# Performance work log

Measured on AMD Instinct MI355X. Metric: run time of the kernel, lower is better.

Reference implementation:

```python
import jax, jax.numpy as jnp
import numpy as np

CI_SCALE = 1.0


def _rot_y(a):
    c, s = np.cos(a), np.sin(a)
    return np.array([[c, 0.0, s], [0.0, 1.0, 0.0], [-s, 0.0, c]], dtype=np.float32)


def setup_inputs() -> dict:
    key = jax.random.key(0)
    B, V, C, Hs, Ws = 1, 3, 32, 256, 256
    Ht, Wt, D = 128, 128, 48
    src_feat = jax.random.normal(key, (B, V, C, Hs, Ws), dtype=jnp.float32)
    # Realistic pinhole cameras so the plane-sweep warp lands in-frame.
    Ks = np.array([[200.0, 0.0, Ws / 2], [0.0, 200.0, Hs / 2], [0.0, 0.0, 1.0]], dtype=np.float32)
    Kt = np.array([[100.0, 0.0, Wt / 2], [0.0, 100.0, Ht / 2], [0.0, 0.0, 1.0]], dtype=np.float32)
    src_exts = np.zeros((B, V, 4, 4), dtype=np.float32)
    for i in range(V):
        R = _rot_y(0.1 * (i - (V - 1) / 2))
        src_exts[0, i, :3, :3] = R
        src_exts[0, i, :3, 3] = np.array([-0.3 * (i - (V - 1) / 2), 0.0, 0.0], dtype=np.float32)
        src_exts[0, i, 3, 3] = 1.0
    tar_exts = np.eye(4, dtype=np.float32)[None]
    return {
        "src_feat": src_feat,
        "src_exts": jnp.asarray(src_exts),
        "src_ints": jnp.asarray(np.broadcast_to(Ks, (B, V, 3, 3)).copy()),
        "tar_exts": jnp.asarray(tar_exts),
        "tar_ints": jnp.asarray(Kt[None].copy()),
        "near_far": jnp.broadcast_to(jnp.array([2.0, 6.0], dtype=jnp.float32).reshape(1, 2, 1, 1), (B, 2, Ht, Wt)),
        "num_depth": D,
    }


def _grid_sample_zeros(feat, grid):
    """Bilinear, padding_mode='zeros', align_corners=False.
    feat: (N,C,Hs,Ws); grid: (N,Hg,Wg,2) normalized -> (N,C,Hg,Wg)."""
    N, C, Hs, Ws = feat.shape
    gx = jnp.clip((grid[..., 0] + 1.0) * (Ws / 2) - 0.5, -1e6, 1e6)
    gy = jnp.clip((grid[..., 1] + 1.0) * (Hs / 2) - 0.5, -1e6, 1e6)
    x0f, y0f = jnp.floor(gx), jnp.floor(gy)
    wx, wy = gx - x0f, gy - y0f
    x0, y0 = x0f.astype(jnp.int32), y0f.astype(jnp.int32)
    x1, y1 = x0 + 1, y0 + 1
    b = jnp.arange(N)[:, None, None]

    def tap(yi, xi):
        valid = (xi >= 0) & (xi < Ws) & (yi >= 0) & (yi < Hs)
        v = feat[b, :, jnp.clip(yi, 0, Hs - 1), jnp.clip(xi, 0, Ws - 1)]  # (N,Hg,Wg,C)
        return v * valid[..., None]

    out = (tap(y0, x0) * ((1 - wy) * (1 - wx))[..., None]
           + tap(y0, x1) * ((1 - wy) * wx)[..., None]
           + tap(y1, x0) * (wy * (1 - wx))[..., None]
           + tap(y1, x1) * (wy * wx)[..., None])
    return jnp.transpose(out, (0, 3, 1, 2))


def _build_feature_volume(src_feat, src_exts, src_ints, tar_exts, tar_ints, depth_values):
    B, V, C, Hs, Ws = src_feat.shape
    D, Ht, Wt = depth_values.shape[1:]
    src_projs = src_ints @ src_exts[..., :3, :]                       # (B,V,3,4)
    tar34 = tar_ints @ tar_exts[:, :3, :]                             # (B,3,4)
    bottom = jnp.broadcast_to(jnp.array([0.0, 0.0, 0.0, 1.0], dtype=tar34.dtype).reshape(1, 1, 4), (B, 1, 4))
    tar_proj = jnp.concatenate([tar34, bottom], axis=1)               # (B,4,4)
    proj = (src_projs @ jnp.linalg.inv(tar_proj)[:, None]).reshape(B * V, 3, 4)
    xs = jnp.arange(Wt, dtype=src_feat.dtype) + 0.5
    ys = jnp.arange(Ht, dtype=src_feat.dtype) + 0.5
    gx, gy = jnp.meshgrid(xs, ys, indexing='xy')                      # (Ht,Wt)
    xyz = jnp.stack([gx, gy, jnp.ones_like(gx)], 0).reshape(3, Ht * Wt)
    dvals = jnp.broadcast_to(depth_values.reshape(B, 1, D, Ht * Wt), (B, V, D, Ht * Wt)).reshape(B * V, 1, D, Ht * Wt)
    p = proj[:, :, :3] @ xyz                                          # (BV,3,HW)
    p = p[:, :, None, :] * dvals + proj[:, :, 3:, None]               # (BV,3,D,HW)
    p = jnp.transpose(p, (0, 2, 3, 1))                                # (BV,D,HW,3)
    z = jnp.maximum(p[..., 2:3], 1e-6)
    g = p[..., :2] / z
    grid = jnp.stack([2 * g[..., 0] / Ws - 1, 2 * g[..., 1] / Hs - 1], -1)  # (BV,D,HW,2)
    warped = _grid_sample_zeros(src_feat.reshape(B * V, C, Hs, Ws), grid)   # (BV,C,D,HW)
    warped = warped.reshape(B, V, C, D, Ht, Wt)
    return jnp.var(warped, axis=1)                                    # (B,C,D,Ht,Wt), unbiased=False


def reference(src_feat, src_exts, src_ints, tar_exts, tar_ints, near_far, num_depth):
    B, _, Ht, Wt = near_far.shape
    t = jnp.linspace(0.0, 1.0, num_depth, dtype=near_far.dtype).reshape(1, num_depth, 1, 1)
    depth_values = near_far[:, :1] + (near_far[:, -1:] - near_far[:, :1]) * t   # (B,D,Ht,Wt)
    vol = _build_feature_volume(src_feat, src_exts, src_ints, tar_exts, tar_ints, depth_values)
    prob = jax.nn.softmax(-vol.mean(axis=1), axis=1)                  # (B,D,Ht,Wt)
    depth = jnp.sum(prob * depth_values, axis=1, keepdims=True)       # (B,1,Ht,Wt)
    var = jnp.sum(prob * jnp.square(depth_values - depth), axis=1, keepdims=True)
    half_ci = CI_SCALE * jnp.sqrt(jnp.maximum(var, 1e-12))
    ci = jnp.concatenate([jnp.maximum(depth - half_ci, depth_values[:, :1]),
                          jnp.minimum(depth + half_ci, depth_values[:, -1:])], axis=1)
    return depth, ci
```

## Files before the change

### kernel.cpp

```cpp
#include <hip/hip_runtime.h>
#include <math.h>

#define NV 3
#define NC 32
#define HS 256
#define WS 256
#define HT 128
#define WT 128
#define ND 48
#define NPIX (HT*WT)
#define HSP 259
#define WSP 259
#define ROW4 (WSP*8)
#define IMG4 (HSP*ROW4)
#define FEAT_T_ELEMS (NV*IMG4*4)
#define NB_INTERIOR (NV*HS)
#define NBORDER_PIX (3*(3*WSP + 3*HS))
#define NBORDER_F4  (NBORDER_PIX*8)
#define NB_BORDER   145

__device__ __forceinline__ float dpp_sum8(float x) {
    int v;
    v = __builtin_amdgcn_update_dpp(0, __float_as_int(x), 0xB1,  0xF, 0xF, true);
    x += __int_as_float(v);
    v = __builtin_amdgcn_update_dpp(0, __float_as_int(x), 0x4E,  0xF, 0xF, true);
    x += __int_as_float(v);
    v = __builtin_amdgcn_update_dpp(0, __float_as_int(x), 0x141, 0xF, 0xF, true);
    x += __int_as_float(v);
    return x;
}
__device__ __forceinline__ float dpp_max8(float x) {
    int v;
    v = __builtin_amdgcn_update_dpp(0, __float_as_int(x), 0xB1,  0xF, 0xF, true);
    x = fmaxf(x, __int_as_float(v));
    v = __builtin_amdgcn_update_dpp(0, __float_as_int(x), 0x4E,  0xF, 0xF, true);
    x = fmaxf(x, __int_as_float(v));
    v = __builtin_amdgcn_update_dpp(0, __float_as_int(x), 0x141, 0xF, 0xF, true);
    x = fmaxf(x, __int_as_float(v));
    return x;
}

__global__ __launch_bounds__(256) void prep(
        const float* __restrict__ src, float* __restrict__ dstf,
        const float* __restrict__ src_exts,
        const float* __restrict__ src_ints,
        const float* __restrict__ tar_exts,
        const float* __restrict__ tar_ints,
        float* __restrict__ proj_out) {
    float4* dst = (float4*)dstf;
    int bid = blockIdx.x;
    if (bid < NB_INTERIOR) {
        int v  = bid >> 8;
        int y  = bid & 255;
        int x0 = threadIdx.x & 31;
        int q  = threadIdx.x >> 5;
        const float* in = src + ((size_t)(v*NC + q*4))*HS*WS + (size_t)y*WS;
        float4* drow = dst + (size_t)(v*HSP + y+1)*ROW4 + 8 + q;
        #pragma unroll
        for (int it = 0; it < 8; it++) {
            int x = it*32 + x0;
            float a = in[x];
            float b = in[HS*WS   + x];
            float c = in[2*HS*WS + x];
            float d = in[3*HS*WS + x];
            drow[x*8] = make_float4(a,b,c,d);
        }
        return;
    }
    int t = (bid - NB_INTERIOR)*256 + threadIdx.x;
    if (t < NBORDER_F4) {
        int pixb = t >> 3, q = t & 7;
        int v = pixb / (NBORDER_PIX/3);
        int r = pixb - v*(NBORDER_PIX/3);
        int y, x;
        if (r < 3*WSP) {
            int band = r / WSP;
            y = (band == 0) ? 0 : (band == 1 ? 257 : 258);
            x = r - band*WSP;
        } else {
            int rr = r - 3*WSP;
            int band = rr >> 8;
            x = (band == 0) ? 0 : (band == 1 ? 257 : 258);
            y = 1 + (rr & 255);
        }
        dst[(v*HSP + y)*WSP*8 + x*8 + q] = make_float4(0.f,0.f,0.f,0.f);
    }
    if (bid == NB_INTERIOR && threadIdx.x == 0) {
        float Kt[9], Et[16];
        for (int i = 0; i < 9;  i++) Kt[i] = tar_ints[i];
        for (int i = 0; i < 16; i++) Et[i] = tar_exts[i];
        float T[12];
        for (int rI = 0; rI < 3; rI++)
            for (int col = 0; col < 4; col++) {
                float s = 0.f;
                for (int k = 0; k < 3; k++) s += Kt[rI*3+k] * Et[k*4+col];
                T[rI*4+col] = s;
            }
        float M[9]  = {T[0],T[1],T[2], T[4],T[5],T[6], T[8],T[9],T[10]};
        float tv[3] = {T[3],T[7],T[11]};
        float det = M[0]*(M[4]*M[8]-M[5]*M[7])
                  - M[1]*(M[3]*M[8]-M[5]*M[6])
                  + M[2]*(M[3]*M[7]-M[4]*M[6]);
        float id = 1.0f/det;
        float Mi[9];
        Mi[0] =  (M[4]*M[8]-M[5]*M[7])*id;
        Mi[1] = -(M[1]*M[8]-M[2]*M[7])*id;
        Mi[2] =  (M[1]*M[5]-M[2]*M[4])*id;
        Mi[3] = -(M[3]*M[8]-M[5]*M[6])*id;
        Mi[4] =  (M[0]*M[8]-M[2]*M[6])*id;
        Mi[5] = -(M[0]*M[5]-M[2]*M[3])*id;
        Mi[6] =  (M[3]*M[7]-M[4]*M[6])*id;
        Mi[7] = -(M[0]*M[7]-M[1]*M[6])*id;
        Mi[8] =  (M[0]*M[4]-M[1]*M[3])*id;
        float mt[3];
        for (int rI = 0; rI < 3; rI++)
            mt[rI] = -(Mi[rI*3+0]*tv[0] + Mi[rI*3+1]*tv[1] + Mi[rI*3+2]*tv[2]);
        float inv4[16] = {Mi[0],Mi[1],Mi[2],mt[0],
                          Mi[3],Mi[4],Mi[5],mt[1],
                          Mi[6],Mi[7],Mi[8],mt[2],
                          0.f,0.f,0.f,1.f};
        for (int v = 0; v < NV; v++) {
            const float* Ks = src_ints + v*9;
            const float* Ev = src_exts + v*16;
            float P34[12];
            for (int rI = 0; rI < 3; rI++)
                for (int col = 0; col < 4; col++) {
                    float s = 0.f;
                    for (int k = 0; k < 3; k++) s += Ks[rI*3+k] * Ev[k*4+col];
                    P34[rI*4+col] = s;
                }
            for (int rI = 0; rI < 3; rI++)
                for (int col = 0; col < 4; col++) {
                    float s = 0.f;
                    for (int k = 0; k < 4; k++) s += P34[rI*4+k] * inv4[k*4+col];
                    proj_out[v*12 + rI*4 + col] = s;
                }
        }
    }
}

__global__ __launch_bounds__(256, 6) void depth_main(
        const float4* __restrict__ featT,
        const float* __restrict__ proj,
        const float* __restrict__ near_far,
        float* __restrict__ out) {
    __shared__ float cl[8][56];

    const int tid  = threadIdx.x;
    const int w    = tid >> 6;
    const int lane = tid & 63;
    const int p    = lane >> 3;
    const int q    = lane & 7;

    const int lb  = ((blockIdx.x & 7) << 8) | (blockIdx.x >> 3);
    const int pix = lb*8 + p;
    const float cx = (pix & (WT-1)) + 0.5f;
    const float cy = (pix >> 7) + 0.5f;

    float rx[NV], ry[NV], rz[NV], tx[NV], ty[NV], tz[NV];
    #pragma unroll
    for (int v = 0; v < NV; v++) {
        const float* P = proj + v*12;
        rx[v] = P[0]*cx + P[1]*cy + P[2];  tx[v] = P[3];
        ry[v] = P[4]*cx + P[5]*cy + P[6];  ty[v] = P[7];
        rz[v] = P[8]*cx + P[9]*cy + P[10]; tz[v] = P[11];
    }

    const float nearv = near_far[pix];
    const float farv  = near_far[NPIX + pix];
    const float step  = (farv - nearv) * (1.0f/(ND-1));
    const float d0    = (float)(w*12);

    const float4* base0 = featT + q;

    #pragma unroll 2
    for (int dd = 0; dd < 12; dd++) {
        const float dv = fmaf(step, d0 + (float)dd, nearv);
        float ax=0.f, ay=0.f, az=0.f, aw=0.f;
        float mxs=0.f, mys=0.f, mzs=0.f, mws=0.f;
        #pragma unroll
        for (int v = 0; v < NV; v++) {
            float pxx = fmaf(rx[v], dv, tx[v]);
            float pyy = fmaf(ry[v], dv, ty[v]);
            float pzz = fmaf(rz[v], dv, tz[v]);
            float z    = fmaxf(pzz, 1e-6f);
            float invz = 1.0f / z;
            float sx = fminf(fmaxf(fmaf(pxx, invz, -0.5f), -1.0f), 256.0f);
            float sy = fminf(fmaxf(fmaf(pyy, invz, -0.5f), -1.0f), 256.0f);
            float x0f = floorf(sx), y0f = floorf(sy);
            float wx = sx - x0f,   wy = sy - y0f;
            int xi = (int)x0f + 1;
            int yi = (int)y0f + 1;
            int r0 = v*IMG4 + yi*ROW4 + xi*8;
            int r1 = r0 + ROW4;
            float4 f00 = base0[r0];
            float4 f01 = base0[r0 + 8];
            float4 f10 = base0[r1];
            float4 f11 = base0[r1 + 8];
            float w11 = wx*wy;
            float w10 = wy - w11;
            float w01 = wx - w11;
            float w00 = (1.0f - wx) - w10;
            float vx = f00.x*w00 + f01.x*w01 + f10.x*w10 + f11.x*w11;
            float vy = f00.y*w00 + f01.y*w01 + f10.y*w10 + f11.y*w11;
            float vz = f00.z*w00 + f01.z*w01 + f10.z*w10 + f11.z*w11;
            float vw = f00.w*w00 + f01.w*w01 + f10.w*w10 + f11.w*w11;
            ax = fmaf(vx,vx,ax); ay = fmaf(vy,vy,ay);
            az = fmaf(vz,vz,az); aw = fmaf(vw,vw,aw);
            mxs += vx; mys += vy; mzs += vz; mws += vw;
        }
        float a  = dpp_sum8((ax + ay) + (az + aw));
        float m2 = dpp_sum8(mxs*mxs + mys*mys + mzs*mzs + mws*mws);
        float cost = (a*(1.0f/3.0f) - m2*(1.0f/9.0f)) * (1.0f/32.0f);
        if (q == 0) cl[p][w*12 + dd] = cost;
    }

    __syncthreads();
    if (w != 0) return;

    float n[6], dvs[6];
    #pragma unroll
    for (int j = 0; j < 6; j++) {
        n[j]   = -cl[p][q + 8*j];
        dvs[j] = fmaf(step, (float)(q + 8*j), nearv);
    }
    float mx = n[0];
    #pragma unroll
    for (int j = 1; j < 6; j++) mx = fmaxf(mx, n[j]);
    mx = dpp_max8(mx);
    float e[6];
    float s0 = 0.f, s1 = 0.f;
    #pragma unroll
    for (int j = 0; j < 6; j++) {
        e[j] = __expf(n[j] - mx);
        s0 += e[j];
        s1 = fmaf(e[j], dvs[j], s1);
    }
    s0 = dpp_sum8(s0);
    s1 = dpp_sum8(s1);
    float depth = s1 / s0;
    float s2 = 0.f;
    #pragma unroll
    for (int j = 0; j < 6; j++) {
        float qd = dvs[j] - depth;
        s2 = fmaf(e[j]*qd, qd, s2);
    }
    s2 = dpp_sum8(s2);
    float var = s2 / s0;
    float hci = sqrtf(fmaxf(var, 1e-12f));
    if (q == 0) {
        out[pix]          = depth;
        out[NPIX + pix]   = fmaxf(depth - hci, nearv);
        out[2*NPIX + pix] = fminf(depth + hci, farv);
    }
}

extern "C" void kernel_launch(void* const* d_in, const int* in_sizes, int n_in,
                              void* d_out, int out_size, void* d_ws, size_t ws_size,
                              hipStream_t stream) {
    const float* src_feat = (const float*)d_in[0];
    const float* src_exts = (const float*)d_in[1];
    const float* src_ints = (const float*)d_in[2];
    const float* tar_exts = (const float*)d_in[3];
    const float* tar_ints = (const float*)d_in[4];
    const float* near_far = (const float*)d_in[5];
    float* out   = (float*)d_out;
    float* featT = (float*)d_ws;
    float* proj  = featT + FEAT_T_ELEMS;

    hipLaunchKernelGGL(prep, dim3(NB_INTERIOR + NB_BORDER), dim3(256), 0, stream,
                       src_feat, featT, src_exts, src_ints, tar_exts, tar_ints, proj);
    hipLaunchKernelGGL(depth_main, dim3(NPIX/8), dim3(256), 0, stream,
                       (const float4*)featT, proj, near_far, out);
}
```

Measured before the change: 123.9 us.

## Use four lanes per pixel with eight channels each in depth kernel

The depth kernel now maps 4 lanes to each pixel, with each lane gathering two adjacent float4s per bilinear tap, so it handles 16 pixels per block. This cuts the DPP reduction steps and raises per-lane ILP, but costs more registers, so the launch bounds drop from 6 to 4 blocks. The softmax stage now reads 12 depth costs per lane. The prep transpose remaps threads so that consecutive lanes write consecutive float4s. The division is replaced by a hardware reciprocal.

```diff
diff --git a/kernel.cpp b/kernel.cpp
--- a/kernel.cpp
+++ b/kernel.cpp
@@ -19,23 +19,19 @@
 #define NBORDER_F4  (NBORDER_PIX*8)
 #define NB_BORDER   145
 
-__device__ __forceinline__ float dpp_sum8(float x) {
+__device__ __forceinline__ float dpp_sum4(float x) {
     int v;
-    v = __builtin_amdgcn_update_dpp(0, __float_as_int(x), 0xB1,  0xF, 0xF, true);
+    v = __builtin_amdgcn_update_dpp(0, __float_as_int(x), 0xB1, 0xF, 0xF, true);
     x += __int_as_float(v);
-    v = __builtin_amdgcn_update_dpp(0, __float_as_int(x), 0x4E,  0xF, 0xF, true);
-    x += __int_as_float(v);
-    v = __builtin_amdgcn_update_dpp(0, __float_as_int(x), 0x141, 0xF, 0xF, true);
+    v = __builtin_amdgcn_update_dpp(0, __float_as_int(x), 0x4E, 0xF, 0xF, true);
     x += __int_as_float(v);
     return x;
 }
-__device__ __forceinline__ float dpp_max8(float x) {
+__device__ __forceinline__ float dpp_max4(float x) {
     int v;
-    v = __builtin_amdgcn_update_dpp(0, __float_as_int(x), 0xB1,  0xF, 0xF, true);
+    v = __builtin_amdgcn_update_dpp(0, __float_as_int(x), 0xB1, 0xF, 0xF, true);
     x = fmaxf(x, __int_as_float(v));
-    v = __builtin_amdgcn_update_dpp(0, __float_as_int(x), 0x4E,  0xF, 0xF, true);
-    x = fmaxf(x, __int_as_float(v));
-    v = __builtin_amdgcn_update_dpp(0, __float_as_int(x), 0x141, 0xF, 0xF, true);
+    v = __builtin_amdgcn_update_dpp(0, __float_as_int(x), 0x4E, 0xF, 0xF, true);
     x = fmaxf(x, __int_as_float(v));
     return x;
 }
@@ -52,13 +48,13 @@
     if (bid < NB_INTERIOR) {
         int v  = bid >> 8;
         int y  = bid & 255;
-        int x0 = threadIdx.x & 31;
-        int q  = threadIdx.x >> 5;
+        int q  = threadIdx.x & 7;
+        int xl = threadIdx.x >> 3;
         const float* in = src + ((size_t)(v*NC + q*4))*HS*WS + (size_t)y*WS;
         float4* drow = dst + (size_t)(v*HSP + y+1)*ROW4 + 8 + q;
         #pragma unroll
         for (int it = 0; it < 8; it++) {
-            int x = it*32 + x0;
+            int x = it*32 + xl;
             float a = in[x];
             float b = in[HS*WS   + x];
             float c = in[2*HS*WS + x];
@@ -139,21 +135,21 @@
     }
 }
 
-__global__ __launch_bounds__(256, 6) void depth_main(
+__global__ __launch_bounds__(256, 4) void depth_main(
         const float4* __restrict__ featT,
         const float* __restrict__ proj,
         const float* __restrict__ near_far,
         float* __restrict__ out) {
-    __shared__ float cl[8][56];
+    __shared__ float cl[16][52];
 
     const int tid  = threadIdx.x;
     const int w    = tid >> 6;
     const int lane = tid & 63;
-    const int p    = lane >> 3;
-    const int q    = lane & 7;
-
-    const int lb  = ((blockIdx.x & 7) << 8) | (blockIdx.x >> 3);
-    const int pix = lb*8 + p;
+    const int p    = lane >> 2;
+    const int q    = lane & 3;
+
+    const int lb  = ((blockIdx.x & 7) << 7) | (blockIdx.x >> 3);
+    const int pix = lb*16 + p;
     const float cx = (pix & (WT-1)) + 0.5f;
     const float cy = (pix >> 7) + 0.5f;
 
@@ -171,46 +167,59 @@
     const float step  = (farv - nearv) * (1.0f/(ND-1));
     const float d0    = (float)(w*12);
 
-    const float4* base0 = featT + q;
+    const float4* baseL = featT + (ROW4 + 8) + 2*q;
 
     #pragma unroll 2
     for (int dd = 0; dd < 12; dd++) {
         const float dv = fmaf(step, d0 + (float)dd, nearv);
-        float ax=0.f, ay=0.f, az=0.f, aw=0.f;
-        float mxs=0.f, mys=0.f, mzs=0.f, mws=0.f;
+        float a0=0.f,a1=0.f,a2=0.f,a3=0.f,a4=0.f,a5=0.f,a6=0.f,a7=0.f;
+        float m0=0.f,m1=0.f,m2_=0.f,m3=0.f,m4=0.f,m5=0.f,m6=0.f,m7=0.f;
         #pragma unroll
         for (int v = 0; v < NV; v++) {
             float pxx = fmaf(rx[v], dv, tx[v]);
             float pyy = fmaf(ry[v], dv, ty[v]);
             float pzz = fmaf(rz[v], dv, tz[v]);
-            float z    = fmaxf(pzz, 1e-6f);
-            float invz = 1.0f / z;
+            float invz = __builtin_amdgcn_rcpf(fmaxf(pzz, 1e-6f));
             float sx = fminf(fmaxf(fmaf(pxx, invz, -0.5f), -1.0f), 256.0f);
             float sy = fminf(fmaxf(fmaf(pyy, invz, -0.5f), -1.0f), 256.0f);
             float x0f = floorf(sx), y0f = floorf(sy);
             float wx = sx - x0f,   wy = sy - y0f;
-            int xi = (int)x0f + 1;
-            int yi = (int)y0f + 1;
+            int xi = (int)x0f;
+            int yi = (int)y0f;
             int r0 = v*IMG4 + yi*ROW4 + xi*8;
             int r1 = r0 + ROW4;
-            float4 f00 = base0[r0];
-            float4 f01 = base0[r0 + 8];
-            float4 f10 = base0[r1];
-            float4 f11 = base0[r1 + 8];
+            float4 fa00 = baseL[r0];
+            float4 fb00 = baseL[r0 + 1];
+            float4 fa01 = baseL[r0 + 8];
+            float4 fb01 = baseL[r0 + 9];
+            float4 fa10 = baseL[r1];
+            float4 fb10 = baseL[r1 + 1];
+            float4 fa11 = baseL[r1 + 8];
+            float4 fb11 = baseL[r1 + 9];
             float w11 = wx*wy;
             float w10 = wy - w11;
             float w01 = wx - w11;
             float w00 = (1.0f - wx) - w10;
-            float vx = f00.x*w00 + f01.x*w01 + f10.x*w10 + f11.x*w11;
-            float vy = f00.y*w00 + f01.y*w01 + f10.y*w10 + f11.y*w11;
-            float vz = f00.z*w00 + f01.z*w01 + f10.z*w10 + f11.z*w11;
-            float vw = f00.w*w00 + f01.w*w01 + f10.w*w10 + f11.w*w11;
-            ax = fmaf(vx,vx,ax); ay = fmaf(vy,vy,ay);
-            az = fmaf(vz,vz,az); aw = fmaf(vw,vw,aw);
-            mxs += vx; mys += vy; mzs += vz; mws += vw;
-        }
-        float a  = dpp_sum8((ax + ay) + (az + aw));
-        float m2 = dpp_sum8(mxs*mxs + mys*mys + mzs*mzs + mws*mws);
+            float v0 = fa00.x*w00 + fa01.x*w01 + fa10.x*w10 + fa11.x*w11;
+            float v1 = fa00.y*w00 + fa01.y*w01 + fa10.y*w10 + fa11.y*w11;
+            float v2 = fa00.z*w00 + fa01.z*w01 + fa10.z*w10 + fa11.z*w11;
+            float v3 = fa00.w*w00 + fa01.w*w01 + fa10.w*w10 + fa11.w*w11;
+            float v4 = fb00.x*w00 + fb01.x*w01 + fb10.x*w10 + fb11.x*w11;
+            float v5 = fb00.y*w00 + fb01.y*w01 + fb10.y*w10 + fb11.y*w11;
+            float v6 = fb00.z*w00 + fb01.z*w01 + fb10.z*w10 + fb11.z*w11;
+            float v7 = fb00.w*w00 + fb01.w*w01 + fb10.w*w10 + fb11.w*w11;
+            a0 = fmaf(v0,v0,a0); a1 = fmaf(v1,v1,a1);
+            a2 = fmaf(v2,v2,a2); a3 = fmaf(v3,v3,a3);
+            a4 = fmaf(v4,v4,a4); a5 = fmaf(v5,v5,a5);
+            a6 = fmaf(v6,v6,a6); a7 = fmaf(v7,v7,a7);
+            m0 += v0; m1 += v1; m2_ += v2; m3 += v3;
+            m4 += v4; m5 += v5; m6  += v6; m7 += v7;
+        }
+        float a  = ((a0+a1)+(a2+a3)) + ((a4+a5)+(a6+a7));
+        float m2 = ((m0*m0 + m1*m1) + (m2_*m2_ + m3*m3))
+                 + ((m4*m4 + m5*m5) + (m6*m6 + m7*m7));
+        a  = dpp_sum4(a);
+        m2 = dpp_sum4(m2);
         float cost = (a*(1.0f/3.0f) - m2*(1.0f/9.0f)) * (1.0f/32.0f);
         if (q == 0) cl[p][w*12 + dd] = cost;
     }
@@ -218,34 +227,31 @@
     __syncthreads();
     if (w != 0) return;
 
-    float n[6], dvs[6];
-    #pragma unroll
-    for (int j = 0; j < 6; j++) {
-        n[j]   = -cl[p][q + 8*j];
-        dvs[j] = fmaf(step, (float)(q + 8*j), nearv);
-    }
+    float n[12], e[12];
+    #pragma unroll
+    for (int j = 0; j < 12; j++) n[j] = -cl[p][q*12 + j];
     float mx = n[0];
     #pragma unroll
-    for (int j = 1; j < 6; j++) mx = fmaxf(mx, n[j]);
-    mx = dpp_max8(mx);
-    float e[6];
+    for (int j = 1; j < 12; j++) mx = fmaxf(mx, n[j]);
+    mx = dpp_max4(mx);
     float s0 = 0.f, s1 = 0.f;
     #pragma unroll
-    for (int j = 0; j < 6; j++) {
+    for (int j = 0; j < 12; j++) {
+        float dvj = fmaf(step, (float)(q*12 + j), nearv);
         e[j] = __expf(n[j] - mx);
         s0 += e[j];
-        s1 = fmaf(e[j], dvs[j], s1);
-    }
-    s0 = dpp_sum8(s0);
-    s1 = dpp_sum8(s1);
+        s1 = fmaf(e[j], dvj, s1);
+    }
+    s0 = dpp_sum4(s0);
+    s1 = dpp_sum4(s1);
     float depth = s1 / s0;
     float s2 = 0.f;
     #pragma unroll
-    for (int j = 0; j < 6; j++) {
-        float qd = dvs[j] - depth;
+    for (int j = 0; j < 12; j++) {
+        float qd = fmaf(step, (float)(q*12 + j), nearv) - depth;
         s2 = fmaf(e[j]*qd, qd, s2);
     }
-    s2 = dpp_sum8(s2);
+    s2 = dpp_sum4(s2);
     float var = s2 / s0;
     float hci = sqrtf(fmaxf(var, 1e-12f));
     if (q == 0) {
@@ -270,6 +276,6 @@
 
     hipLaunchKernelGGL(prep, dim3(NB_INTERIOR + NB_BORDER), dim3(256), 0, stream,
                        src_feat, featT, src_exts, src_ints, tar_exts, tar_ints, proj);
-    hipLaunchKernelGGL(depth_main, dim3(NPIX/8), dim3(256), 0, stream,
+    hipLaunchKernelGGL(depth_main, dim3(NPIX/16), dim3(256), 0, stream,
                        (const float4*)featT, proj, near_far, out);
 }
```

Result: slower. 131.0 us (+5.8%).
